# Kernel optimization log

Hardware: AMD Instinct MI355X
Metric: run time of the kernel (lower is better)

The kernel has to match this reference:

```python
import jax, jax.numpy as jnp
import numpy as np

B, S, HID = 1, 2048, 4096
NH, NKV, D = 32, 8, 128          # query heads, kv heads, head_dim
GROUPS = NH // NKV               # GQA repeat factor = 4
WINDOW = 1024                    # sliding-window size
ROPE_BASE = 10000.0


def setup_inputs() -> dict:
    key = jax.random.key(0)
    k = jax.random.split(key, 5)
    hidden_states = jax.random.normal(k[0], (B, S, HID), jnp.float32)
    Wq = jax.random.normal(k[1], (HID, HID), jnp.float32) * 0.02
    Wk = jax.random.normal(k[2], (NKV * D, HID), jnp.float32) * 0.02
    Wv = jax.random.normal(k[3], (NKV * D, HID), jnp.float32) * 0.02
    Wo = jax.random.normal(k[4], (HID, HID), jnp.float32) * 0.02
    position_ids = jnp.arange(S, dtype=jnp.int64 if jax.config.jax_enable_x64 else jnp.int32)[None, :]
    # Sliding-window causal additive mask [B,1,S,S]: key j visible to query i iff i-WINDOW < j <= i
    i = jnp.arange(S)
    visible = (i[None, :] <= i[:, None]) & (i[:, None] - i[None, :] < WINDOW)
    neg = jnp.finfo(jnp.float32).min
    attention_mask = jnp.where(visible, 0.0, neg)[None, None, :, :].astype(jnp.float32)
    return {"hidden_states": hidden_states, "attention_mask": attention_mask,
            "position_ids": position_ids, "Wq": Wq, "Wk": Wk, "Wv": Wv, "Wo": Wo}


def _rotate_half(x):
    x1, x2 = x[..., : D // 2], x[..., D // 2:]
    return jnp.concatenate((-x2, x1), axis=-1)


def _rope_cos_sin(position_ids, dtype):
    # inv_freq over even dims; gather-by-position_ids == direct indexing
    inv_freq = 1.0 / (ROPE_BASE ** (jnp.arange(0, D, 2, dtype=jnp.float32) / D))  # [D/2]
    freqs = position_ids.astype(jnp.float32)[..., None] * inv_freq                # [B,S,D/2]
    emb = jnp.concatenate((freqs, freqs), axis=-1)                                # [B,S,D]
    cos = jnp.cos(emb)[:, None, :, :].astype(dtype)                               # [B,1,S,D]
    sin = jnp.sin(emb)[:, None, :, :].astype(dtype)
    return cos, sin


def reference(hidden_states, attention_mask, position_ids, Wq, Wk, Wv, Wo):
    bsz, q_len, _ = hidden_states.shape
    # projections (nn.Linear: y = x @ W.T)
    q = (hidden_states @ Wq.T).reshape(bsz, q_len, NH, D).transpose(0, 2, 1, 3)    # [B,NH,S,D]
    k = (hidden_states @ Wk.T).reshape(bsz, q_len, NKV, D).transpose(0, 2, 1, 3)   # [B,NKV,S,D]
    v = (hidden_states @ Wv.T).reshape(bsz, q_len, NKV, D).transpose(0, 2, 1, 3)
    cos, sin = _rope_cos_sin(position_ids, q.dtype)
    q = q * cos + _rotate_half(q) * sin
    k = k * cos + _rotate_half(k) * sin
    # GQA repeat_kv (repeat_interleave along head dim)
    k = jnp.repeat(k, GROUPS, axis=1)                                              # [B,NH,S,D]
    v = jnp.repeat(v, GROUPS, axis=1)
    scores = jnp.einsum('bhqd,bhkd->bhqk', q, k) / np.sqrt(D)                       # [B,NH,S,S]
    scores = scores + attention_mask
    scores = jnp.maximum(scores, jnp.finfo(scores.dtype).min)
    probs = jax.nn.softmax(scores.astype(jnp.float32), axis=-1).astype(q.dtype)
    out = jnp.einsum('bhqk,bhkd->bhqd', probs, v)                                   # [B,NH,S,D]
    out = out.transpose(0, 2, 1, 3).reshape(bsz, q_len, HID)
    return out @ Wo.T
```

## Files before the change

### kernel.cpp

```cpp
#include <hip/hip_runtime.h>

#define S_LEN 2048
#define HID   4096
#define NH    32
#define NKV   8
#define DH    128
#define KVD   (NKV*DH)
#define WIN   1024
#define NTOT  6144

typedef __bf16 bf16_t;
typedef __bf16 bfrag  __attribute__((ext_vector_type(8)));
typedef __bf16 bf4    __attribute__((ext_vector_type(4)));
typedef float  ffrag  __attribute__((ext_vector_type(4)));
typedef float  facc   __attribute__((ext_vector_type(16)));

__global__ __launch_bounds__(256) void f32_to_bf16_kernel(const float* __restrict__ src,
                                                          bf16_t* __restrict__ dst, int n4) {
  int i = blockIdx.x * 256 + threadIdx.x;
  if (i < n4) {
    ffrag v = *(const ffrag*)(src + (size_t)i * 4);
    bf4 o;
    o[0] = (bf16_t)v[0]; o[1] = (bf16_t)v[1]; o[2] = (bf16_t)v[2]; o[3] = (bf16_t)v[3];
    *(bf4*)(dst + (size_t)i * 4) = o;
  }
}

__global__ __launch_bounds__(256) void cvt4_kernel(const float* __restrict__ h,
    const float* __restrict__ Wq, const float* __restrict__ Wk, const float* __restrict__ Wv,
    bf16_t* __restrict__ hB, bf16_t* __restrict__ WqB,
    bf16_t* __restrict__ WkB, bf16_t* __restrict__ WvB) {
  int i = blockIdx.x * 256 + threadIdx.x;
  const int N0 = S_LEN * HID / 4;
  const int N1 = N0 + HID * HID / 4;
  const int N2 = N1 + KVD * HID / 4;
  const float* s; bf16_t* d; int off;
  if (i < N0)      { s = h;  d = hB;  off = i; }
  else if (i < N1) { s = Wq; d = WqB; off = i - N0; }
  else if (i < N2) { s = Wk; d = WkB; off = i - N1; }
  else             { s = Wv; d = WvB; off = i - N2; }
  ffrag v = *(const ffrag*)(s + (size_t)off * 4);
  bf4 o;
  o[0] = (bf16_t)v[0]; o[1] = (bf16_t)v[1]; o[2] = (bf16_t)v[2]; o[3] = (bf16_t)v[3];
  *(bf4*)(d + (size_t)off * 4) = o;
}

__global__ __launch_bounds__(256) void rope_table_kernel(float2* __restrict__ tab) {
  int i = blockIdx.x * 256 + threadIdx.x;
  int s = i >> 6, d = i & 63;
  float inv = exp2f((float)d * (-13.287712379549449f / 64.f));
  float ang = (float)s * inv;
  tab[i] = make_float2(cosf(ang), sinf(ang));
}

__device__ __forceinline__ void load_lds16(const bf16_t* g, bf16_t* l) {
  __builtin_amdgcn_global_load_lds((__attribute__((address_space(1))) void*)g,
                                   (__attribute__((address_space(3))) void*)l,
                                   16, 0, 0);
}

#define BARW() asm volatile("s_barrier" ::: "memory")
#define WAITV(n) asm volatile("s_waitcnt vmcnt(" #n ")" ::: "memory")
#define LGKM0() do { asm volatile("s_waitcnt lgkmcnt(0)" ::: "memory"); \
                     __builtin_amdgcn_sched_barrier(0); } while (0)

template <int BNR, int OUT_MODE>
__device__ __forceinline__ void gemm16_body(const bf16_t* __restrict__ A,
                                            const bf16_t* __restrict__ B,
                                            void* __restrict__ Cv,
                                            int N, bf16_t* lds) {
  constexpr int K     = 4096;
  constexpr int NT    = K / 64;
  constexpr int NTF   = BNR / 64;
  constexpr int WC    = BNR / 4;
  constexpr int ABUFE = 128 * 64;
  constexpr int BBUFE = BNR * 64;

  bf16_t* As0 = lds;
  bf16_t* Bs0 = lds + 2 * ABUFE;

  const int raw  = blockIdx.x;
  const int xcd  = raw & 7;
  const int slot = raw >> 3;
  const int bx   = xcd * 4 + (slot & 3);
  const int by   = slot >> 2;
  const int row0 = by * 128;
  const int col0 = bx * BNR;

  const int tid  = threadIdx.x;
  const int wave = tid >> 6;
  const int lane = tid & 63;
  const int wr = wave >> 2, wc = wave & 3;
  const int n = lane & 15, qd = lane >> 4;

  const int rsub = tid >> 3;
  const int sg   = (tid & 7) ^ (rsub & 7);
  const bf16_t* Ag = A + (size_t)(row0 + rsub) * K + sg * 8;
  const bf16_t* Bg = B + (size_t)(col0 + rsub) * K + sg * 8;
  const int wbase = wave * 512;

  const int pg0 = ( qd      ^ (n & 7)) * 8;
  const int pg1 = ((4 | qd) ^ (n & 7)) * 8;
  const int abase = (wr * 64 + n) * 64;
  const int bbase = (wc * WC + n) * 64;

  ffrag acc[4][NTF];
#pragma unroll
  for (int mt = 0; mt < 4; ++mt)
#pragma unroll
    for (int nt = 0; nt < NTF; ++nt) {
      acc[mt][nt][0] = 0.f; acc[mt][nt][1] = 0.f; acc[mt][nt][2] = 0.f; acc[mt][nt][3] = 0.f;
    }

  auto STAGE = [&](int t, int s) {
    const int ko = t * 64;
    bf16_t* as = As0 + s * ABUFE + wbase;
    bf16_t* bs = Bs0 + s * BBUFE + wbase;
    load_lds16(Ag + ko, as);
    load_lds16(Ag + (size_t)64 * K + ko, as + 4096);
    load_lds16(Bg + ko, bs);
    load_lds16(Bg + (size_t)64 * K + ko, bs + 4096);
    if constexpr (BNR == 192) load_lds16(Bg + (size_t)128 * K + ko, bs + 8192);
  };

  STAGE(0, 0); STAGE(1, 1);
  if constexpr (BNR == 192) { WAITV(5); } else { WAITV(4); }
  BARW();

  for (int t = 0; t < NT; ++t) {
    const int s = t & 1;
    const bf16_t* Asl = As0 + s * ABUFE;
    const bf16_t* Bsl = Bs0 + s * BBUFE;
    bfrag av[4], bv[NTF];

#pragma unroll
    for (int mt = 0; mt < 4; ++mt) av[mt] = *(const bfrag*)(Asl + abase + mt * 1024 + pg0);
#pragma unroll
    for (int nt = 0; nt < NTF; ++nt) bv[nt] = *(const bfrag*)(Bsl + bbase + nt * 1024 + pg0);
    __builtin_amdgcn_s_setprio(1);
#pragma unroll
    for (int mt = 0; mt < 4; ++mt)
#pragma unroll
      for (int nt = 0; nt < NTF; ++nt)
        acc[mt][nt] = __builtin_amdgcn_mfma_f32_16x16x32_bf16(av[mt], bv[nt], acc[mt][nt], 0, 0, 0);
    __builtin_amdgcn_s_setprio(0);

#pragma unroll
    for (int mt = 0; mt < 4; ++mt) av[mt] = *(const bfrag*)(Asl + abase + mt * 1024 + pg1);
#pragma unroll
    for (int nt = 0; nt < NTF; ++nt) bv[nt] = *(const bfrag*)(Bsl + bbase + nt * 1024 + pg1);
    __builtin_amdgcn_s_setprio(1);
#pragma unroll
    for (int mt = 0; mt < 4; ++mt)
#pragma unroll
      for (int nt = 0; nt < NTF; ++nt)
        acc[mt][nt] = __builtin_amdgcn_mfma_f32_16x16x32_bf16(av[mt], bv[nt], acc[mt][nt], 0, 0, 0);
    __builtin_amdgcn_s_setprio(0);

    LGKM0();
    BARW();
    if (t + 2 < NT) STAGE(t + 2, s);
    if (t + 1 < NT) {
      if (t + 2 < NT) { if constexpr (BNR == 192) { WAITV(5); } else { WAITV(4); } }
      else            { WAITV(0); }
      BARW();
    }
  }

  const int orow = row0 + wr * 64 + qd * 4;
  const int ocol = col0 + wc * WC + n;
#pragma unroll
  for (int mt = 0; mt < 4; ++mt)
#pragma unroll
    for (int nt = 0; nt < NTF; ++nt)
#pragma unroll
      for (int r = 0; r < 4; ++r) {
        size_t idx = (size_t)(orow + mt * 16 + r) * N + (ocol + nt * 16);
        if (OUT_MODE == 1) ((bf16_t*)Cv)[idx] = (bf16_t)acc[mt][nt][r];
        else               ((float*)Cv)[idx]  = acc[mt][nt][r];
      }
}

__global__ __launch_bounds__(512, 4) void gemm_qkv_kernel(const bf16_t* __restrict__ hB,
                                                          const bf16_t* __restrict__ Wqkv,
                                                          bf16_t* __restrict__ C) {
  __shared__ __align__(16) bf16_t lds[2 * 128 * 64 + 2 * 192 * 64];
  gemm16_body<192, 1>(hB, Wqkv, C, NTOT, lds);
}

template <int BN, int OUT_MODE>
__device__ __forceinline__ void gemm32_body(const bf16_t* __restrict__ A,
                                            const bf16_t* __restrict__ B,
                                            void* __restrict__ Cv,
                                            int row0, int col0,
                                            int N, bf16_t* lds) {
  constexpr int K     = 4096;
  constexpr int NT    = K / 64;
  constexpr int NB    = BN / 64;
  constexpr int WCOL  = BN / 2;
  constexpr int BSW   = BN / 32;
  constexpr int ABUFE = 128 * 64;
  constexpr int BBUFE = BN * 64;

  bf16_t* As0 = lds;
  bf16_t* Bs0 = lds + 2 * ABUFE;

  const int tid  = threadIdx.x;
  const int wave = tid >> 6;
  const int lane = tid & 63;
  const int wm = wave >> 1, wn = wave & 1;
  const int l31 = lane & 31, hi = lane >> 5, l7 = lane & 7;

  const int rsub = tid >> 3;
  const int sg   = (tid & 7) ^ (rsub & 7);
  const bf16_t* Ag = A + (size_t)(row0 + rsub) * K + sg * 8;
  const bf16_t* Bg = B + (size_t)(col0 + rsub) * K + sg * 8;
  const int wbase = wave * 512;

  int pgk[4];
#pragma unroll
  for (int ks = 0; ks < 4; ++ks) pgk[ks] = ((ks * 2 + hi) ^ l7) * 8;
  const int aoff = (wm * 64 + l31) * 64;
  const int boff = (wn * WCOL + l31) * 64;

  facc acc[2][NB];
#pragma unroll
  for (int mt = 0; mt < 2; ++mt)
#pragma unroll
    for (int nt = 0; nt < NB; ++nt)
#pragma unroll
      for (int j = 0; j < 16; ++j) acc[mt][nt][j] = 0.f;

  auto STAGE = [&](int t, int s) {
    const int ko = t * 64;
    bf16_t* as = As0 + s * ABUFE + wbase;
    bf16_t* bs = Bs0 + s * BBUFE + wbase;
#pragma unroll
    for (int i = 0; i < 4; ++i)
      load_lds16(Ag + (size_t)(i * 32) * K + ko, as + i * 2048);
#pragma unroll
    for (int i = 0; i < BSW; ++i)
      load_lds16(Bg + (size_t)(i * 32) * K + ko, bs + i * 2048);
  };

  STAGE(0, 0); STAGE(1, 1);
  WAITV(8);
  BARW();

  for (int t = 0; t < NT; ++t) {
    const int s = t & 1;
    const bf16_t* Asl = As0 + s * ABUFE;
    const bf16_t* Bsl = Bs0 + s * BBUFE;

#pragma unroll
    for (int ks = 0; ks < 4; ++ks) {
      bfrag av0 = *(const bfrag*)(Asl + aoff + pgk[ks]);
      bfrag av1 = *(const bfrag*)(Asl + aoff + 2048 + pgk[ks]);
      bfrag bv[NB];
#pragma unroll
      for (int nt = 0; nt < NB; ++nt)
        bv[nt] = *(const bfrag*)(Bsl + boff + nt * 2048 + pgk[ks]);
      __builtin_amdgcn_s_setprio(1);
#pragma unroll
      for (int nt = 0; nt < NB; ++nt)
        acc[0][nt] = __builtin_amdgcn_mfma_f32_32x32x16_bf16(av0, bv[nt], acc[0][nt], 0, 0, 0);
#pragma unroll
      for (int nt = 0; nt < NB; ++nt)
        acc[1][nt] = __builtin_amdgcn_mfma_f32_32x32x16_bf16(av1, bv[nt], acc[1][nt], 0, 0, 0);
      __builtin_amdgcn_s_setprio(0);
    }

    LGKM0();
    BARW();
    if (t + 2 < NT) STAGE(t + 2, s);
    if (t + 1 < NT) {
      if (t + 2 < NT) { WAITV(8); }
      else            { WAITV(0); }
      BARW();
    }
  }

  const int orow = row0 + wm * 64 + 4 * hi;
  const int ocol = col0 + wn * WCOL + l31;
#pragma unroll
  for (int mt = 0; mt < 2; ++mt)
#pragma unroll
    for (int nt = 0; nt < NB; ++nt)
#pragma unroll
      for (int j = 0; j < 16; ++j) {
        int r = orow + mt * 32 + (j & 3) + 8 * (j >> 2);
        size_t idx = (size_t)r * N + (ocol + nt * 32);
        if (OUT_MODE == 1) ((bf16_t*)Cv)[idx] = (bf16_t)acc[mt][nt][j];
        else               ((float*)Cv)[idx]  = acc[mt][nt][j];
      }
}

__global__ __launch_bounds__(256, 2) void gemm_out_kernel(const bf16_t* __restrict__ A,
                                                          const bf16_t* __restrict__ B,
                                                          float* __restrict__ out) {
  __shared__ __align__(16) bf16_t lds[2 * 128 * 64 + 2 * 128 * 64];
  const int raw  = blockIdx.x;
  const int xcd  = raw & 7;
  const int slot = raw >> 3;
  const int bx   = xcd * 4 + (slot & 3);
  const int by   = slot >> 2;
  gemm32_body<128, 0>(A, B, out, by * 128, bx * 128, HID, lds);
}

__global__ __launch_bounds__(256) void ropecvt_kernel(const bf16_t* __restrict__ Cqkv,
                                                      const float2* __restrict__ tab,
                                                      bf16_t* __restrict__ Qb,
                                                      bf16_t* __restrict__ Kb,
                                                      bf16_t* __restrict__ Vb) {
  int idx = blockIdx.x * 256 + threadIdx.x;
  int g  = idx & 7;
  int t  = idx >> 3;
  int hh = t % 48;
  int s  = t / 48;
  const bf16_t* r0 = Cqkv + (size_t)s * NTOT + hh * 128;
  bfrag a0 = *(const bfrag*)&r0[g * 8];
  bfrag a1 = *(const bfrag*)&r0[g * 8 + 64];
  bf16_t* p;
  bool rope;
  if (hh < NH)           { p = Qb + (size_t)s * HID + hh * DH;        rope = true; }
  else if (hh < NH+NKV)  { p = Kb + (size_t)s * KVD + (hh - NH) * DH; rope = true; }
  else                   { p = Vb + (size_t)s * KVD + (hh - 40) * DH; rope = false; }
  bfrag o1, o2;
  if (rope) {
    const float2* tb = tab + s * 64 + g * 8;
#pragma unroll
    for (int j = 0; j < 8; ++j) {
      float x1 = (float)a0[j];
      float x2 = (float)a1[j];
      float2 cs = tb[j];
      o1[j] = (bf16_t)(x1 * cs.x - x2 * cs.y);
      o2[j] = (bf16_t)(x2 * cs.x + x1 * cs.y);
    }
  } else {
#pragma unroll
    for (int j = 0; j < 8; ++j) { o1[j] = a0[j]; o2[j] = a1[j]; }
  }
  *(bfrag*)&p[g * 8]      = o1;
  *(bfrag*)&p[g * 8 + 64] = o2;
}

#define KS_STRIDE 136
#define VT_STRIDE 72
#define PS_STRIDE 72

__global__ __launch_bounds__(256, 3) void attn_kernel(const bf16_t* __restrict__ Q,
                                                      const bf16_t* __restrict__ Kc,
                                                      const bf16_t* __restrict__ Vc,
                                                      bf16_t* __restrict__ AO) {
  const int qt   = 31 - blockIdx.x;
  const int h    = blockIdx.y;
  const int kvh  = h >> 2;
  const int q0   = qt * 64;
  const int tid  = threadIdx.x;
  const int wq   = tid >> 6;
  const int lane = tid & 63;
  const int n    = lane & 15;
  const int quad = lane >> 4;
  const float scale = 0.08838834764831845f;

  __shared__ __align__(16) bf16_t Ks[64 * KS_STRIDE];
  __shared__ __align__(16) bf16_t VT[128 * VT_STRIDE];
  __shared__ __align__(16) bf16_t Ps[4][16 * PS_STRIDE];

  bfrag aq[4];
#pragma unroll
  for (int kc = 0; kc < 4; ++kc) {
    bfrag t = *(const bfrag*)&Q[(size_t)(q0 + wq * 16 + n) * HID + h * DH + kc * 32 + quad * 8];
#pragma unroll
    for (int e = 0; e < 8; ++e) t[e] = (bf16_t)((float)t[e] * scale);
    aq[kc] = t;
  }

  ffrag acc[8];
#pragma unroll
  for (int dt = 0; dt < 8; ++dt) { acc[dt][0] = 0.f; acc[dt][1] = 0.f; acc[dt][2] = 0.f; acc[dt][3] = 0.f; }
  float lrow[4] = {0.f, 0.f, 0.f, 0.f};

  const int ktlo = (q0 >= WIN) ? ((q0 - (WIN - 1)) >> 6) : 0;
  const int kthi = (q0 + 63) >> 6;

  const int kg = tid & 15;
  const int dg = tid >> 4;

  bfrag pk[4], pv[4];
  {
    const int k0 = ktlo * 64;
#pragma unroll
    for (int i = 0; i < 4; ++i) {
      int pos = i * 256 + tid;
      pk[i] = *(const bfrag*)&Kc[(size_t)(k0 + (pos >> 4)) * KVD + kvh * DH + (pos & 15) * 8];
    }
#pragma unroll
    for (int j = 0; j < 4; ++j)
      pv[j] = *(const bfrag*)&Vc[(size_t)(k0 + j * 16 + kg) * KVD + kvh * DH + dg * 8];
  }

  for (int kt = ktlo; kt <= kthi; ++kt) {
    const int k0 = kt * 64;
    __syncthreads();
#pragma unroll
    for (int i = 0; i < 4; ++i) {
      int pos = i * 256 + tid;
      *(bfrag*)&Ks[(pos >> 4) * KS_STRIDE + (pos & 15) * 8] = pk[i];
    }
#pragma unroll
    for (int i = 0; i < 8; ++i) {
      bf4 pkk;
      pkk[0] = pv[0][i]; pkk[1] = pv[1][i]; pkk[2] = pv[2][i]; pkk[3] = pv[3][i];
      *(bf4*)&VT[(dg * 8 + i) * VT_STRIDE + kg * 4] = pkk;
    }
    __syncthreads();
    if (kt < kthi) {
      const int k1 = k0 + 64;
#pragma unroll
      for (int i = 0; i < 4; ++i) {
        int pos = i * 256 + tid;
        pk[i] = *(const bfrag*)&Kc[(size_t)(k1 + (pos >> 4)) * KVD + kvh * DH + (pos & 15) * 8];
      }
#pragma unroll
      for (int j = 0; j < 4; ++j)
        pv[j] = *(const bfrag*)&Vc[(size_t)(k1 + j * 16 + kg) * KVD + kvh * DH + dg * 8];
    }

    ffrag s[4];
#pragma unroll
    for (int nt = 0; nt < 4; ++nt) { s[nt][0] = 0.f; s[nt][1] = 0.f; s[nt][2] = 0.f; s[nt][3] = 0.f; }
#pragma unroll
    for (int kc = 0; kc < 4; ++kc) {
      bfrag bk[4];
#pragma unroll
      for (int nt = 0; nt < 4; ++nt)
        bk[nt] = *(const bfrag*)&Ks[(nt * 16 + n) * KS_STRIDE + kc * 32 + quad * 8];
      __builtin_amdgcn_s_setprio(1);
#pragma unroll
      for (int nt = 0; nt < 4; ++nt)
        s[nt] = __builtin_amdgcn_mfma_f32_16x16x32_bf16(aq[kc], bk[nt], s[nt], 0, 0, 0);
      __builtin_amdgcn_s_setprio(0);
    }

    const bool full = (k0 + 63 <= q0) && (q0 + 63 - k0 < WIN);
    if (!full) {
#pragma unroll
      for (int nt = 0; nt < 4; ++nt)
#pragma unroll
        for (int r = 0; r < 4; ++r) {
          int q = q0 + wq * 16 + quad * 4 + r;
          int k = k0 + nt * 16 + n;
          bool vis = (k <= q) && ((q - k) < WIN);
          if (!vis) s[nt][r] = -1e30f;
        }
    }

#pragma unroll
    for (int r = 0; r < 4; ++r) {
      bf4 pkk;
      float ps0 = __expf(s[0][r]);
      float ps1 = __expf(s[1][r]);
      float ps2 = __expf(s[2][r]);
      float ps3 = __expf(s[3][r]);
      lrow[r] += (ps0 + ps1) + (ps2 + ps3);
      pkk[0] = (bf16_t)ps0; pkk[1] = (bf16_t)ps1; pkk[2] = (bf16_t)ps2; pkk[3] = (bf16_t)ps3;
      *(bf4*)&Ps[wq][(quad * 4 + r) * PS_STRIDE + n * 4] = pkk;
    }

#pragma unroll
    for (int kc = 0; kc < 2; ++kc) {
      bfrag ap = *(const bfrag*)&Ps[wq][n * PS_STRIDE + kc * 32 + quad * 8];
#pragma unroll
      for (int dt = 0; dt < 8; dt += 4) {
        bfrag bv0 = *(const bfrag*)&VT[((dt + 0) * 16 + n) * VT_STRIDE + kc * 32 + quad * 8];
        bfrag bv1 = *(const bfrag*)&VT[((dt + 1) * 16 + n) * VT_STRIDE + kc * 32 + quad * 8];
        bfrag bv2 = *(const bfrag*)&VT[((dt + 2) * 16 + n) * VT_STRIDE + kc * 32 + quad * 8];
        bfrag bv3 = *(const bfrag*)&VT[((dt + 3) * 16 + n) * VT_STRIDE + kc * 32 + quad * 8];
        __builtin_amdgcn_s_setprio(1);
        acc[dt + 0] = __builtin_amdgcn_mfma_f32_16x16x32_bf16(ap, bv0, acc[dt + 0], 0, 0, 0);
        acc[dt + 1] = __builtin_amdgcn_mfma_f32_16x16x32_bf16(ap, bv1, acc[dt + 1], 0, 0, 0);
        acc[dt + 2] = __builtin_amdgcn_mfma_f32_16x16x32_bf16(ap, bv2, acc[dt + 2], 0, 0, 0);
        acc[dt + 3] = __builtin_amdgcn_mfma_f32_16x16x32_bf16(ap, bv3, acc[dt + 3], 0, 0, 0);
        __builtin_amdgcn_s_setprio(0);
      }
    }
  }

#pragma unroll
  for (int off = 1; off < 16; off <<= 1)
#pragma unroll
    for (int r = 0; r < 4; ++r) lrow[r] += __shfl_xor(lrow[r], off);
  float inv[4];
#pragma unroll
  for (int r = 0; r < 4; ++r) inv[r] = 1.f / lrow[r];
#pragma unroll
  for (int dt = 0; dt < 8; ++dt)
#pragma unroll
    for (int r = 0; r < 4; ++r)
      AO[(size_t)(q0 + wq * 16 + quad * 4 + r) * HID + h * DH + dt * 16 + n] =
          (bf16_t)(acc[dt][r] * inv[r]);
}

extern "C" void kernel_launch(void* const* d_in, const int* in_sizes, int n_in,
                              void* d_out, int out_size, void* d_ws, size_t ws_size,
                              hipStream_t stream) {
  const float* h  = (const float*)d_in[0];
  const float* Wq = (const float*)d_in[3];
  const float* Wk = (const float*)d_in[4];
  const float* Wv = (const float*)d_in[5];
  const float* Wo = (const float*)d_in[6];
  float* out = (float*)d_out;

  char* ws = (char*)d_ws;
  const size_t MB = (size_t)1 << 20;
  bf16_t* hB    = (bf16_t*)(ws + 0 * MB);
  bf16_t* Qb    = (bf16_t*)(ws + 0 * MB);
  bf16_t* WqB   = (bf16_t*)(ws + 16 * MB);
  bf16_t* WkB   = (bf16_t*)(ws + 48 * MB);
  bf16_t* WvB   = (bf16_t*)(ws + 56 * MB);
  bf16_t* Cqkv  = (bf16_t*)(ws + 64 * MB);
  float2* Rtab  = (float2*)(ws + 88 * MB);
  bf16_t* WoB   = (bf16_t*)(ws + 64 * MB);
  bf16_t* AOb   = (bf16_t*)(ws + 96 * MB);
  bf16_t* Kb    = (bf16_t*)(ws + 112 * MB);
  bf16_t* Vb    = (bf16_t*)(ws + 116 * MB);

  rope_table_kernel<<<(S_LEN * 64) / 256, 256, 0, stream>>>(Rtab);

  cvt4_kernel<<<(S_LEN * HID + HID * HID + 2 * KVD * HID) / 4 / 256, 256, 0, stream>>>(
      h, Wq, Wk, Wv, hB, WqB, WkB, WvB);

  gemm_qkv_kernel<<<512, 512, 0, stream>>>(hB, WqB, Cqkv);

  ropecvt_kernel<<<(S_LEN * 48 * 8) / 256, 256, 0, stream>>>(Cqkv, Rtab, Qb, Kb, Vb);

  f32_to_bf16_kernel<<<(HID * HID / 4 + 255) / 256, 256, 0, stream>>>(Wo, WoB, HID * HID / 4);

  attn_kernel<<<dim3(32, NH), 256, 0, stream>>>(Qb, Kb, Vb, AOb);

  gemm_out_kernel<<<512, 256, 0, stream>>>(AOb, WoB, out);
}
```

Baseline: 452.7 us.

## Fuse fp32-to-bf16 weight conversion into QKV and output GEMM B-tile loads

Removes the standalone conversion passes for Wq/Wk/Wv/Wo and instead has each GEMM load fp32 weight rows into registers, convert them to bf16, and write them swizzled into LDS, double-buffered one stage ahead. This eliminates a large write-then-reread of converted weights in global memory and two kernel launches. In exchange, the GEMMs read twice as many bytes for B per tile, re-read across row blocks, and hold more registers for the prefetched fp32 data, which may lower occupancy or expose load latency.

```diff
diff --git a/kernel.cpp b/kernel.cpp
--- a/kernel.cpp
+++ b/kernel.cpp
@@ -15,34 +15,13 @@
 typedef float  ffrag  __attribute__((ext_vector_type(4)));
 typedef float  facc   __attribute__((ext_vector_type(16)));
 
-__global__ __launch_bounds__(256) void f32_to_bf16_kernel(const float* __restrict__ src,
-                                                          bf16_t* __restrict__ dst, int n4) {
+__global__ __launch_bounds__(256) void cvt_h_kernel(const float* __restrict__ h,
+                                                    bf16_t* __restrict__ hB) {
   int i = blockIdx.x * 256 + threadIdx.x;
-  if (i < n4) {
-    ffrag v = *(const ffrag*)(src + (size_t)i * 4);
-    bf4 o;
-    o[0] = (bf16_t)v[0]; o[1] = (bf16_t)v[1]; o[2] = (bf16_t)v[2]; o[3] = (bf16_t)v[3];
-    *(bf4*)(dst + (size_t)i * 4) = o;
-  }
-}
-
-__global__ __launch_bounds__(256) void cvt4_kernel(const float* __restrict__ h,
-    const float* __restrict__ Wq, const float* __restrict__ Wk, const float* __restrict__ Wv,
-    bf16_t* __restrict__ hB, bf16_t* __restrict__ WqB,
-    bf16_t* __restrict__ WkB, bf16_t* __restrict__ WvB) {
-  int i = blockIdx.x * 256 + threadIdx.x;
-  const int N0 = S_LEN * HID / 4;
-  const int N1 = N0 + HID * HID / 4;
-  const int N2 = N1 + KVD * HID / 4;
-  const float* s; bf16_t* d; int off;
-  if (i < N0)      { s = h;  d = hB;  off = i; }
-  else if (i < N1) { s = Wq; d = WqB; off = i - N0; }
-  else if (i < N2) { s = Wk; d = WkB; off = i - N1; }
-  else             { s = Wv; d = WvB; off = i - N2; }
-  ffrag v = *(const ffrag*)(s + (size_t)off * 4);
+  ffrag v = *(const ffrag*)(h + (size_t)i * 4);
   bf4 o;
   o[0] = (bf16_t)v[0]; o[1] = (bf16_t)v[1]; o[2] = (bf16_t)v[2]; o[3] = (bf16_t)v[3];
-  *(bf4*)(d + (size_t)off * 4) = o;
+  *(bf4*)(hB + (size_t)i * 4) = o;
 }
 
 __global__ __launch_bounds__(256) void rope_table_kernel(float2* __restrict__ tab) {
@@ -64,18 +43,23 @@
 #define LGKM0() do { asm volatile("s_waitcnt lgkmcnt(0)" ::: "memory"); \
                      __builtin_amdgcn_sched_barrier(0); } while (0)
 
-template <int BNR, int OUT_MODE>
-__device__ __forceinline__ void gemm16_body(const bf16_t* __restrict__ A,
-                                            const bf16_t* __restrict__ B,
-                                            void* __restrict__ Cv,
-                                            int N, bf16_t* lds) {
+__device__ __forceinline__ bfrag cvt8(const float4& a, const float4& b) {
+  bfrag w;
+  w[0] = (bf16_t)a.x; w[1] = (bf16_t)a.y; w[2] = (bf16_t)a.z; w[3] = (bf16_t)a.w;
+  w[4] = (bf16_t)b.x; w[5] = (bf16_t)b.y; w[6] = (bf16_t)b.z; w[7] = (bf16_t)b.w;
+  return w;
+}
+
+__global__ __launch_bounds__(512, 4) void gemm_qkv_kernel(const bf16_t* __restrict__ hB,
+                                                          const float* __restrict__ Wq,
+                                                          const float* __restrict__ Wk,
+                                                          const float* __restrict__ Wv,
+                                                          bf16_t* __restrict__ C) {
   constexpr int K     = 4096;
   constexpr int NT    = K / 64;
-  constexpr int NTF   = BNR / 64;
-  constexpr int WC    = BNR / 4;
   constexpr int ABUFE = 128 * 64;
-  constexpr int BBUFE = BNR * 64;
-
+  constexpr int BBUFE = 192 * 64;
+  __shared__ __align__(16) bf16_t lds[2 * ABUFE + 2 * BBUFE];
   bf16_t* As0 = lds;
   bf16_t* Bs0 = lds + 2 * ABUFE;
 
@@ -85,7 +69,7 @@
   const int bx   = xcd * 4 + (slot & 3);
   const int by   = slot >> 2;
   const int row0 = by * 128;
-  const int col0 = bx * BNR;
+  const int col0 = bx * 192;
 
   const int tid  = threadIdx.x;
   const int wave = tid >> 6;
@@ -94,116 +78,136 @@
   const int n = lane & 15, qd = lane >> 4;
 
   const int rsub = tid >> 3;
-  const int sg   = (tid & 7) ^ (rsub & 7);
-  const bf16_t* Ag = A + (size_t)(row0 + rsub) * K + sg * 8;
-  const bf16_t* Bg = B + (size_t)(col0 + rsub) * K + sg * 8;
+  const int gA   = (tid & 7) ^ (rsub & 7);
+  const bf16_t* Ag = hB + (size_t)(row0 + rsub) * K + gA * 8;
   const int wbase = wave * 512;
+
+  const int gB   = tid & 7;
+  const float* Bgf[3];
+#pragma unroll
+  for (int i = 0; i < 3; ++i) {
+    int r = col0 + rsub + i * 64;
+    Bgf[i] = (r < HID) ? (Wq + (size_t)r * K)
+           : (r < HID + KVD) ? (Wk + (size_t)(r - HID) * K)
+                             : (Wv + (size_t)(r - HID - KVD) * K);
+  }
+  const int bwoff = rsub * 64 + ((gB ^ (rsub & 7)) * 8);
 
   const int pg0 = ( qd      ^ (n & 7)) * 8;
   const int pg1 = ((4 | qd) ^ (n & 7)) * 8;
   const int abase = (wr * 64 + n) * 64;
-  const int bbase = (wc * WC + n) * 64;
-
-  ffrag acc[4][NTF];
+  const int bbase = (wc * 48 + n) * 64;
+
+  ffrag acc[4][3];
 #pragma unroll
   for (int mt = 0; mt < 4; ++mt)
 #pragma unroll
-    for (int nt = 0; nt < NTF; ++nt) {
+    for (int nt = 0; nt < 3; ++nt) {
       acc[mt][nt][0] = 0.f; acc[mt][nt][1] = 0.f; acc[mt][nt][2] = 0.f; acc[mt][nt][3] = 0.f;
     }
 
-  auto STAGE = [&](int t, int s) {
+  float4 breg[2][3][2];
+
+  auto STAGE_A = [&](int t, int s) {
     const int ko = t * 64;
     bf16_t* as = As0 + s * ABUFE + wbase;
-    bf16_t* bs = Bs0 + s * BBUFE + wbase;
     load_lds16(Ag + ko, as);
     load_lds16(Ag + (size_t)64 * K + ko, as + 4096);
-    load_lds16(Bg + ko, bs);
-    load_lds16(Bg + (size_t)64 * K + ko, bs + 4096);
-    if constexpr (BNR == 192) load_lds16(Bg + (size_t)128 * K + ko, bs + 8192);
   };
-
-  STAGE(0, 0); STAGE(1, 1);
-  if constexpr (BNR == 192) { WAITV(5); } else { WAITV(4); }
+  auto LOADB = [&](int t) {
+    const int ko = t * 64 + gB * 8;
+    const int p  = t & 1;
+#pragma unroll
+    for (int i = 0; i < 3; ++i) {
+      breg[p][i][0] = *(const float4*)(Bgf[i] + ko);
+      breg[p][i][1] = *(const float4*)(Bgf[i] + ko + 4);
+    }
+  };
+  auto WRITEB = [&](int t, int s) {
+    const int p = t & 1;
+    bf16_t* bs = Bs0 + s * BBUFE;
+#pragma unroll
+    for (int i = 0; i < 3; ++i)
+      *(bfrag*)&bs[i * 4096 + bwoff] = cvt8(breg[p][i][0], breg[p][i][1]);
+  };
+
+  STAGE_A(0, 0); LOADB(0);
+  WAITV(0);
+  WRITEB(0, 0);
+  STAGE_A(1, 1); LOADB(1);
+  LGKM0();
   BARW();
 
   for (int t = 0; t < NT; ++t) {
     const int s = t & 1;
     const bf16_t* Asl = As0 + s * ABUFE;
     const bf16_t* Bsl = Bs0 + s * BBUFE;
-    bfrag av[4], bv[NTF];
+    bfrag av[4], bv[3];
 
 #pragma unroll
     for (int mt = 0; mt < 4; ++mt) av[mt] = *(const bfrag*)(Asl + abase + mt * 1024 + pg0);
 #pragma unroll
-    for (int nt = 0; nt < NTF; ++nt) bv[nt] = *(const bfrag*)(Bsl + bbase + nt * 1024 + pg0);
+    for (int nt = 0; nt < 3; ++nt) bv[nt] = *(const bfrag*)(Bsl + bbase + nt * 1024 + pg0);
     __builtin_amdgcn_s_setprio(1);
 #pragma unroll
     for (int mt = 0; mt < 4; ++mt)
 #pragma unroll
-      for (int nt = 0; nt < NTF; ++nt)
+      for (int nt = 0; nt < 3; ++nt)
         acc[mt][nt] = __builtin_amdgcn_mfma_f32_16x16x32_bf16(av[mt], bv[nt], acc[mt][nt], 0, 0, 0);
     __builtin_amdgcn_s_setprio(0);
 
 #pragma unroll
     for (int mt = 0; mt < 4; ++mt) av[mt] = *(const bfrag*)(Asl + abase + mt * 1024 + pg1);
 #pragma unroll
-    for (int nt = 0; nt < NTF; ++nt) bv[nt] = *(const bfrag*)(Bsl + bbase + nt * 1024 + pg1);
+    for (int nt = 0; nt < 3; ++nt) bv[nt] = *(const bfrag*)(Bsl + bbase + nt * 1024 + pg1);
     __builtin_amdgcn_s_setprio(1);
 #pragma unroll
     for (int mt = 0; mt < 4; ++mt)
 #pragma unroll
-      for (int nt = 0; nt < NTF; ++nt)
+      for (int nt = 0; nt < 3; ++nt)
         acc[mt][nt] = __builtin_amdgcn_mfma_f32_16x16x32_bf16(av[mt], bv[nt], acc[mt][nt], 0, 0, 0);
     __builtin_amdgcn_s_setprio(0);
 
     LGKM0();
     BARW();
-    if (t + 2 < NT) STAGE(t + 2, s);
+    if (t + 2 < NT) { STAGE_A(t + 2, s); LOADB(t + 2); }
     if (t + 1 < NT) {
-      if (t + 2 < NT) { if constexpr (BNR == 192) { WAITV(5); } else { WAITV(4); } }
-      else            { WAITV(0); }
+      if (t + 2 < NT) { WAITV(8); } else { WAITV(0); }
+      WRITEB(t + 1, s ^ 1);
+      LGKM0();
       BARW();
     }
   }
 
   const int orow = row0 + wr * 64 + qd * 4;
-  const int ocol = col0 + wc * WC + n;
+  const int ocol = col0 + wc * 48 + n;
 #pragma unroll
   for (int mt = 0; mt < 4; ++mt)
 #pragma unroll
-    for (int nt = 0; nt < NTF; ++nt)
-#pragma unroll
-      for (int r = 0; r < 4; ++r) {
-        size_t idx = (size_t)(orow + mt * 16 + r) * N + (ocol + nt * 16);
-        if (OUT_MODE == 1) ((bf16_t*)Cv)[idx] = (bf16_t)acc[mt][nt][r];
-        else               ((float*)Cv)[idx]  = acc[mt][nt][r];
-      }
-}
-
-__global__ __launch_bounds__(512, 4) void gemm_qkv_kernel(const bf16_t* __restrict__ hB,
-                                                          const bf16_t* __restrict__ Wqkv,
-                                                          bf16_t* __restrict__ C) {
-  __shared__ __align__(16) bf16_t lds[2 * 128 * 64 + 2 * 192 * 64];
-  gemm16_body<192, 1>(hB, Wqkv, C, NTOT, lds);
-}
-
-template <int BN, int OUT_MODE>
-__device__ __forceinline__ void gemm32_body(const bf16_t* __restrict__ A,
-                                            const bf16_t* __restrict__ B,
-                                            void* __restrict__ Cv,
-                                            int row0, int col0,
-                                            int N, bf16_t* lds) {
+    for (int nt = 0; nt < 3; ++nt)
+#pragma unroll
+      for (int r = 0; r < 4; ++r)
+        C[(size_t)(orow + mt * 16 + r) * NTOT + (ocol + nt * 16)] = (bf16_t)acc[mt][nt][r];
+}
+
+__global__ __launch_bounds__(256, 2) void gemm_out_kernel(const bf16_t* __restrict__ A,
+                                                          const float* __restrict__ Wo,
+                                                          float* __restrict__ out) {
   constexpr int K     = 4096;
   constexpr int NT    = K / 64;
-  constexpr int NB    = BN / 64;
-  constexpr int WCOL  = BN / 2;
-  constexpr int BSW   = BN / 32;
   constexpr int ABUFE = 128 * 64;
-  constexpr int BBUFE = BN * 64;
-
+  constexpr int BBUFE = 128 * 64;
+  __shared__ __align__(16) bf16_t lds[2 * ABUFE + 2 * BBUFE];
   bf16_t* As0 = lds;
   bf16_t* Bs0 = lds + 2 * ABUFE;
+
+  const int raw  = blockIdx.x;
+  const int xcd  = raw & 7;
+  const int slot = raw >> 3;
+  const int bx   = xcd * 4 + (slot & 3);
+  const int by   = slot >> 2;
+  const int row0 = by * 128;
+  const int col0 = bx * 128;
 
   const int tid  = threadIdx.x;
   const int wave = tid >> 6;
@@ -212,39 +216,59 @@
   const int l31 = lane & 31, hi = lane >> 5, l7 = lane & 7;
 
   const int rsub = tid >> 3;
-  const int sg   = (tid & 7) ^ (rsub & 7);
-  const bf16_t* Ag = A + (size_t)(row0 + rsub) * K + sg * 8;
-  const bf16_t* Bg = B + (size_t)(col0 + rsub) * K + sg * 8;
+  const int gA   = (tid & 7) ^ (rsub & 7);
+  const bf16_t* Ag = A + (size_t)(row0 + rsub) * K + gA * 8;
   const int wbase = wave * 512;
+
+  const int gB = tid & 7;
+  const float* Bgf = Wo + (size_t)(col0 + rsub) * K;
+  const int bwoff = rsub * 64 + ((gB ^ (rsub & 7)) * 8);
 
   int pgk[4];
 #pragma unroll
   for (int ks = 0; ks < 4; ++ks) pgk[ks] = ((ks * 2 + hi) ^ l7) * 8;
   const int aoff = (wm * 64 + l31) * 64;
-  const int boff = (wn * WCOL + l31) * 64;
-
-  facc acc[2][NB];
+  const int boff = (wn * 64 + l31) * 64;
+
+  facc acc[2][2];
 #pragma unroll
   for (int mt = 0; mt < 2; ++mt)
 #pragma unroll
-    for (int nt = 0; nt < NB; ++nt)
+    for (int nt = 0; nt < 2; ++nt)
 #pragma unroll
       for (int j = 0; j < 16; ++j) acc[mt][nt][j] = 0.f;
 
-  auto STAGE = [&](int t, int s) {
+  float4 breg[2][4][2];
+
+  auto STAGE_A = [&](int t, int s) {
     const int ko = t * 64;
     bf16_t* as = As0 + s * ABUFE + wbase;
-    bf16_t* bs = Bs0 + s * BBUFE + wbase;
 #pragma unroll
     for (int i = 0; i < 4; ++i)
       load_lds16(Ag + (size_t)(i * 32) * K + ko, as + i * 2048);
-#pragma unroll
-    for (int i = 0; i < BSW; ++i)
-      load_lds16(Bg + (size_t)(i * 32) * K + ko, bs + i * 2048);
   };
-
-  STAGE(0, 0); STAGE(1, 1);
-  WAITV(8);
+  auto LOADB = [&](int t) {
+    const int ko = t * 64 + gB * 8;
+    const int p  = t & 1;
+#pragma unroll
+    for (int i = 0; i < 4; ++i) {
+      breg[p][i][0] = *(const float4*)(Bgf + (size_t)(i * 32) * K + ko);
+      breg[p][i][1] = *(const float4*)(Bgf + (size_t)(i * 32) * K + ko + 4);
+    }
+  };
+  auto WRITEB = [&](int t, int s) {
+    const int p = t & 1;
+    bf16_t* bs = Bs0 + s * BBUFE;
+#pragma unroll
+    for (int i = 0; i < 4; ++i)
+      *(bfrag*)&bs[i * 2048 + bwoff] = cvt8(breg[p][i][0], breg[p][i][1]);
+  };
+
+  STAGE_A(0, 0); LOADB(0);
+  WAITV(0);
+  WRITEB(0, 0);
+  STAGE_A(1, 1); LOADB(1);
+  LGKM0();
   BARW();
 
   for (int t = 0; t < NT; ++t) {
@@ -256,55 +280,38 @@
     for (int ks = 0; ks < 4; ++ks) {
       bfrag av0 = *(const bfrag*)(Asl + aoff + pgk[ks]);
       bfrag av1 = *(const bfrag*)(Asl + aoff + 2048 + pgk[ks]);
-      bfrag bv[NB];
-#pragma unroll
-      for (int nt = 0; nt < NB; ++nt)
-        bv[nt] = *(const bfrag*)(Bsl + boff + nt * 2048 + pgk[ks]);
+      bfrag bv0 = *(const bfrag*)(Bsl + boff + pgk[ks]);
+      bfrag bv1 = *(const bfrag*)(Bsl + boff + 2048 + pgk[ks]);
       __builtin_amdgcn_s_setprio(1);
-#pragma unroll
-      for (int nt = 0; nt < NB; ++nt)
-        acc[0][nt] = __builtin_amdgcn_mfma_f32_32x32x16_bf16(av0, bv[nt], acc[0][nt], 0, 0, 0);
-#pragma unroll
-      for (int nt = 0; nt < NB; ++nt)
-        acc[1][nt] = __builtin_amdgcn_mfma_f32_32x32x16_bf16(av1, bv[nt], acc[1][nt], 0, 0, 0);
+      acc[0][0] = __builtin_amdgcn_mfma_f32_32x32x16_bf16(av0, bv0, acc[0][0], 0, 0, 0);
+      acc[0][1] = __builtin_amdgcn_mfma_f32_32x32x16_bf16(av0, bv1, acc[0][1], 0, 0, 0);
+      acc[1][0] = __builtin_amdgcn_mfma_f32_32x32x16_bf16(av1, bv0, acc[1][0], 0, 0, 0);
+      acc[1][1] = __builtin_amdgcn_mfma_f32_32x32x16_bf16(av1, bv1, acc[1][1], 0, 0, 0);
       __builtin_amdgcn_s_setprio(0);
     }
 
     LGKM0();
     BARW();
-    if (t + 2 < NT) STAGE(t + 2, s);
+    if (t + 2 < NT) { STAGE_A(t + 2, s); LOADB(t + 2); }
     if (t + 1 < NT) {
-      if (t + 2 < NT) { WAITV(8); }
-      else            { WAITV(0); }
+      if (t + 2 < NT) { WAITV(12); } else { WAITV(0); }
+      WRITEB(t + 1, s ^ 1);
+      LGKM0();
       BARW();
     }
   }
 
   const int orow = row0 + wm * 64 + 4 * hi;
-  const int ocol = col0 + wn * WCOL + l31;
+  const int ocol = col0 + wn * 64 + l31;
 #pragma unroll
   for (int mt = 0; mt < 2; ++mt)
 #pragma unroll
-    for (int nt = 0; nt < NB; ++nt)
+    for (int nt = 0; nt < 2; ++nt)
 #pragma unroll
       for (int j = 0; j < 16; ++j) {
         int r = orow + mt * 32 + (j & 3) + 8 * (j >> 2);
-        size_t idx = (size_t)r * N + (ocol + nt * 32);
-        if (OUT_MODE == 1) ((bf16_t*)Cv)[idx] = (bf16_t)acc[mt][nt][j];
-        else               ((float*)Cv)[idx]  = acc[mt][nt][j];
+        out[(size_t)r * HID + (ocol + nt * 32)] = acc[mt][nt][j];
       }
-}
-
-__global__ __launch_bounds__(256, 2) void gemm_out_kernel(const bf16_t* __restrict__ A,
-                                                          const bf16_t* __restrict__ B,
-                                                          float* __restrict__ out) {
-  __shared__ __align__(16) bf16_t lds[2 * 128 * 64 + 2 * 128 * 64];
-  const int raw  = blockIdx.x;
-  const int xcd  = raw & 7;
-  const int slot = raw >> 3;
-  const int bx   = xcd * 4 + (slot & 3);
-  const int by   = slot >> 2;
-  gemm32_body<128, 0>(A, B, out, by * 128, bx * 128, HID, lds);
 }
 
 __global__ __launch_bounds__(256) void ropecvt_kernel(const bf16_t* __restrict__ Cqkv,
@@ -516,28 +523,21 @@
   const size_t MB = (size_t)1 << 20;
   bf16_t* hB    = (bf16_t*)(ws + 0 * MB);
   bf16_t* Qb    = (bf16_t*)(ws + 0 * MB);
-  bf16_t* WqB   = (bf16_t*)(ws + 16 * MB);
-  bf16_t* WkB   = (bf16_t*)(ws + 48 * MB);
-  bf16_t* WvB   = (bf16_t*)(ws + 56 * MB);
   bf16_t* Cqkv  = (bf16_t*)(ws + 64 * MB);
   float2* Rtab  = (float2*)(ws + 88 * MB);
-  bf16_t* WoB   = (bf16_t*)(ws + 64 * MB);
   bf16_t* AOb   = (bf16_t*)(ws + 96 * MB);
   bf16_t* Kb    = (bf16_t*)(ws + 112 * MB);
   bf16_t* Vb    = (bf16_t*)(ws + 116 * MB);
 
   rope_table_kernel<<<(S_LEN * 64) / 256, 256, 0, stream>>>(Rtab);
 
-  cvt4_kernel<<<(S_LEN * HID + HID * HID + 2 * KVD * HID) / 4 / 256, 256, 0, stream>>>(
-      h, Wq, Wk, Wv, hB, WqB, WkB, WvB);
-
-  gemm_qkv_kernel<<<512, 512, 0, stream>>>(hB, WqB, Cqkv);
+  cvt_h_kernel<<<(S_LEN * HID / 4) / 256, 256, 0, stream>>>(h, hB);
+
+  gemm_qkv_kernel<<<512, 512, 0, stream>>>(hB, Wq, Wk, Wv, Cqkv);
 
   ropecvt_kernel<<<(S_LEN * 48 * 8) / 256, 256, 0, stream>>>(Cqkv, Rtab, Qb, Kb, Vb);
 
-  f32_to_bf16_kernel<<<(HID * HID / 4 + 255) / 256, 256, 0, stream>>>(Wo, WoB, HID * HID / 4);
-
   attn_kernel<<<dim3(32, NH), 256, 0, stream>>>(Qb, Kb, Vb, AOb);
 
-  gemm_out_kernel<<<512, 256, 0, stream>>>(AOb, WoB, out);
-}
+  gemm_out_kernel<<<512, 256, 0, stream>>>(AOb, Wo, out);
+}
```

Result: slower. 1.328 ms (+193.3%).
